# Kernel tuning notes

Measured on AMD Instinct MI355X. Metric: run time of the kernel, lower is better.

## Reference

```python
import jax, jax.numpy as jnp
import numpy as np
from jax import lax

# db4 analysis filters (pywt convention)
DEC_LO = np.array([-0.010597401785069032, 0.0328830116668852, 0.030841381835560764,
                   -0.18703481171909309, -0.027983769416859854, 0.6308807679298589,
                   0.7148465705529157, 0.2303778133088965], dtype=np.float32)
DEC_HI = np.array([-0.2303778133088965, 0.7148465705529157, -0.6308807679298589,
                   -0.027983769416859854, 0.18703481171909309, 0.030841381835560764,
                   -0.0328830116668852, -0.010597401785069032], dtype=np.float32)
LF = 8          # db4 filter length
J = 4           # wavelet levels
H = 768         # hidden size per modality
B, S = 8, 2048  # batch, seq len

# pytorch_wavelets cross-correlates with time-reversed dec filters (afb)
H0R = jnp.asarray(DEC_LO[::-1].copy())
H1R = jnp.asarray(DEC_HI[::-1].copy())
# conv_transpose(rec) == cross-correlation with flip(rec); flip(rec)=dec
G0F = jnp.asarray(DEC_LO)
G1F = jnp.asarray(DEC_HI)


def afb1d(x):
    """One analysis level along last axis, zero-pad mode. x: (B, C, N)."""
    b, c, n = x.shape
    outsize = (n + LF - 1) // 2          # pywt.dwt_coeff_len, mode='zero'
    p = 2 * (outsize - 1) - n + LF       # total pad (extra goes on the right)
    kern = jnp.stack([H0R, H1R])[:, None, :]               # (2,1,LF)
    y = lax.conv_general_dilated(x.reshape(b * c, 1, n), kern,
                                 (2,), [(p // 2, p - p // 2)])
    return y[:, 0].reshape(b, c, outsize), y[:, 1].reshape(b, c, outsize)


def sfb1d(lo, hi):
    """One synthesis level (inverse of afb1d). lo, hi: (B, C, N)."""
    b, c, n = lo.shape
    z = jnp.stack([lo.reshape(b * c, n), hi.reshape(b * c, n)], axis=1)  # (BC,2,N)
    kern = jnp.stack([G0F, G1F])[None]                     # (1,2,LF)
    # conv_transpose(stride=2, padding=LF-2) as lhs-dilated cross-correlation
    y = lax.conv_general_dilated(z, kern, (1,), [(1, 1)], lhs_dilation=(2,))
    return y[:, 0].reshape(b, c, 2 * n - LF + 2)


def dwt1d(x):
    highs = []
    lo = x
    for _ in range(J):
        lo, hi = afb1d(lo)
        highs.append(hi)
    return lo, highs


def idwt1d(lo, highs):
    for hi in highs[::-1]:
        if lo.shape[-1] > hi.shape[-1]:   # static shape check (as in IDWT1D)
            lo = lo[..., :-1]
        lo = sfb1d(lo, hi)
    return lo


def setup_inputs() -> dict:
    key = jax.random.key(0)
    k1, k2, k3 = jax.random.split(key, 3)
    x = jax.random.normal(k1, (B, S, 3 * H), dtype=jnp.float32)
    low_w = jax.random.normal(k2, (3, 3, H, H), dtype=jnp.float32) * 0.02
    high_w = jax.random.normal(k3, (3, J, 3, H, H), dtype=jnp.float32) * 0.02
    weight = jnp.ones((3,), dtype=jnp.float32)   # config['initializer_weight']
    return {"x": x, "low_w": low_w, "high_w": high_w, "weight": weight}


def reference(x, low_w, high_w, weight):
    b, s, _ = x.shape
    xs = jnp.stack(jnp.split(x, 3, axis=-1))               # (3,B,S,H) modalities
    xt = xs.transpose(0, 1, 3, 2).reshape(3 * b, H, s)     # DWT along seq axis
    lo, highs = dwt1d(xt)
    lo_s = lo.reshape(3, b, H, -1).transpose(0, 1, 3, 2)           # (3,B,Nl,H)
    hi_s = [h.reshape(3, b, H, -1).transpose(0, 1, 3, 2) for h in highs]

    # cross-modal sigmoid-gated fusion: m = target modal, j = source modal
    g = jnp.einsum('jbnh,mjgh->mjbng', lo_s, low_w)
    fused_l = (jax.nn.sigmoid(g) * lo_s[None]).sum(axis=1)         # (3,B,Nl,H)
    fused_h = []
    for k in range(J):
        gk = jnp.einsum('jbnh,mjgh->mjbng', hi_s[k], high_w[:, k])
        fused_h.append((jax.nn.sigmoid(gk) * hi_s[k][None]).sum(axis=1))

    fl = fused_l.transpose(0, 1, 3, 2).reshape(3 * b, H, -1)
    fh = [f.transpose(0, 1, 3, 2).reshape(3 * b, H, -1) for f in fused_h]
    recon = idwt1d(fl, fh).reshape(3, b, H, s).transpose(0, 1, 3, 2)  # (3,B,S,H)
    return (recon - xs) * weight[:, None, None, None]
```

## Files before the change

kernel.cpp:

```cpp
#include <hip/hip_runtime.h>
#include <hip/hip_bf16.h>

#define H 768
#define NB 8
#define SLEN 2048
#define N1 1027
#define N2 517
#define N3 262
#define N4 134

typedef short bf16x8 __attribute__((ext_vector_type(8)));
typedef float f32x4 __attribute__((ext_vector_type(4)));
typedef unsigned short ushortx4 __attribute__((ext_vector_type(4)));
typedef unsigned short ushortx8 __attribute__((ext_vector_type(8)));

__device__ __forceinline__ float sigmoidf(float v) {
    return 1.0f / (1.0f + __expf(-v));
}

__device__ __forceinline__ unsigned short f2bf(float f) {
    union { float f; unsigned u; } v; v.f = f;
    unsigned r = v.u + 0x7fffu + ((v.u >> 16) & 1u);
    return (unsigned short)(r >> 16);
}

__device__ __forceinline__ float bf2f(unsigned short u) {
    union { unsigned u; float f; } v; v.u = ((unsigned)u) << 16;
    return v.f;
}

__device__ __forceinline__ void gload_lds16(const void* g, void* l) {
    __builtin_amdgcn_global_load_lds(
        (const __attribute__((address_space(1))) unsigned int*)g,
        (__attribute__((address_space(3))) unsigned int*)l,
        16, 0, 0);
}

__global__ __launch_bounds__(192)
void dwt_analysis_kernel(const float* __restrict__ in,
                         float* __restrict__ lo_f32,
                         unsigned short* __restrict__ lo_bf,
                         unsigned short* __restrict__ hi_bf,
                         int n_in, int n_out, int rows_pad,
                         long j_stride, long b_stride, long t_stride)
{
    const float h0r[8] = { 0.2303778133088965f,  0.7148465705529157f,  0.6308807679298589f,
                          -0.027983769416859854f, -0.18703481171909309f, 0.030841381835560764f,
                           0.0328830116668852f, -0.010597401785069032f };
    const float h1r[8] = { -0.010597401785069032f, -0.0328830116668852f, 0.030841381835560764f,
                            0.18703481171909309f, -0.027983769416859854f, -0.6308807679298589f,
                            0.7148465705529157f, -0.2303778133088965f };
    const int tbase = blockIdx.x * 16;
    const int jb = blockIdx.y;
    const int j = jb >> 3, b = jb & 7;
    const int h = threadIdx.x * 4;
    const float* src = in + j * j_stride + b * b_stride + h;
    const float4 z4 = make_float4(0.f, 0.f, 0.f, 0.f);

    float4 w[8];
#pragma unroll
    for (int k = 0; k < 8; ++k) {
        int s = 2 * tbase - 6 + k;
        w[k] = (s >= 0 && s < n_in) ? *(const float4*)(src + (long)s * t_stride) : z4;
    }
#pragma unroll
    for (int tt = 0; tt < 16; ++tt) {
        const int t = tbase + tt;
        if (t < n_out) {
            float lx = 0.f, ly = 0.f, lz = 0.f, lw = 0.f;
            float hx = 0.f, hy = 0.f, hz = 0.f, hw = 0.f;
#pragma unroll
            for (int k = 0; k < 8; ++k) {
                float4 v = w[(2 * tt + k) & 7];
                lx += v.x * h0r[k]; ly += v.y * h0r[k]; lz += v.z * h0r[k]; lw += v.w * h0r[k];
                hx += v.x * h1r[k]; hy += v.y * h1r[k]; hz += v.z * h1r[k]; hw += v.w * h1r[k];
            }
            const long prow = (long)j * rows_pad + b * n_out + t;
            if (lo_f32) {
                float4 o; o.x = lx; o.y = ly; o.z = lz; o.w = lw;
                *(float4*)(lo_f32 + ((long)jb * n_out + t) * H + h) = o;
            }
            if (lo_bf) {
                ushortx4 p; p[0] = f2bf(lx); p[1] = f2bf(ly); p[2] = f2bf(lz); p[3] = f2bf(lw);
                *(ushortx4*)(lo_bf + prow * H + h) = p;
            }
            ushortx4 qv; qv[0] = f2bf(hx); qv[1] = f2bf(hy); qv[2] = f2bf(hz); qv[3] = f2bf(hw);
            *(ushortx4*)(hi_bf + prow * H + h) = qv;
        }
        if (tt < 15) {
            int s0n = 2 * t + 2;
            w[(2 * tt) & 7]     = (s0n     < n_in) ? *(const float4*)(src + (long)s0n * t_stride)       : z4;
            w[(2 * tt + 1) & 7] = (s0n + 1 < n_in) ? *(const float4*)(src + (long)(s0n + 1) * t_stride) : z4;
        }
    }
}

__device__ __forceinline__ void synth_pair(const float4* wl, const float4* wh, int u,
                                           float4* oe, float4* oo)
{
    const float g0[8] = { -0.010597401785069032f, 0.0328830116668852f, 0.030841381835560764f,
                          -0.18703481171909309f, -0.027983769416859854f, 0.6308807679298589f,
                           0.7148465705529157f, 0.2303778133088965f };
    const float g1[8] = { -0.2303778133088965f, 0.7148465705529157f, -0.6308807679298589f,
                          -0.027983769416859854f, 0.18703481171909309f, 0.030841381835560764f,
                          -0.0328830116668852f, -0.010597401785069032f };
    float ex = 0.f, ey = 0.f, ez = 0.f, ew = 0.f;
    float ox = 0.f, oy = 0.f, oz = 0.f, ow = 0.f;
#pragma unroll
    for (int d = 0; d < 4; ++d) {
        float4 vl = wl[(u + d) & 3];
        float4 vh = wh[(u + d) & 3];
        const float cle = g0[2 * d + 1], che = g1[2 * d + 1];
        const float clo = g0[2 * d],     cho = g1[2 * d];
        ex += vl.x * cle + vh.x * che; ey += vl.y * cle + vh.y * che;
        ez += vl.z * cle + vh.z * che; ew += vl.w * cle + vh.w * che;
        ox += vl.x * clo + vh.x * cho; oy += vl.y * clo + vh.y * cho;
        oz += vl.z * clo + vh.z * cho; ow += vl.w * clo + vh.w * cho;
    }
    oe->x = ex; oe->y = ey; oe->z = ez; oe->w = ew;
    oo->x = ox; oo->y = oy; oo->z = oz; oo->w = ow;
}

__global__ __launch_bounds__(192)
void dwt_synth_kernel(const float* __restrict__ lo,
                      const float* __restrict__ hi,
                      float* __restrict__ out,
                      int n, int lo_alloc, int n_out)
{
    const int ubase = blockIdx.x * 16;
    const int mb = blockIdx.y;
    const int h = threadIdx.x * 4;
    const float* lop = lo + (long)mb * lo_alloc * H + h;
    const float* hip_ = hi + (long)mb * n * H + h;
    float* outp = out + (long)mb * n_out * H + h;
    const float4 z4 = make_float4(0.f, 0.f, 0.f, 0.f);

    float4 wl[4], wh[4];
#pragma unroll
    for (int d = 0; d < 4; ++d) {
        int i = ubase + d;
        bool ok = (i < n);
        wl[(ubase + d) & 3] = ok ? *(const float4*)(lop + (long)i * H) : z4;
        wh[(ubase + d) & 3] = ok ? *(const float4*)(hip_ + (long)i * H) : z4;
    }
#pragma unroll
    for (int uu = 0; uu < 16; ++uu) {
        const int u = ubase + uu;
        if (2 * u < n_out) {
            float4 oe, oo;
            synth_pair(wl, wh, u, &oe, &oo);
            *(float4*)(outp + (long)(2 * u) * H) = oe;
            *(float4*)(outp + (long)(2 * u + 1) * H) = oo;
        }
        if (uu < 15) {
            int i = u + 4;
            bool ok = (i < n);
            wl[u & 3] = ok ? *(const float4*)(lop + (long)i * H) : z4;
            wh[u & 3] = ok ? *(const float4*)(hip_ + (long)i * H) : z4;
        }
    }
}

__global__ __launch_bounds__(192)
void dwt_synth_final_kernel(const float* __restrict__ lo,
                            const float* __restrict__ hi,
                            const float* __restrict__ x,
                            const float* __restrict__ weight,
                            float* __restrict__ out,
                            int n, int lo_alloc)
{
    const int ubase = blockIdx.x * 16;
    const int mb = blockIdx.y;
    const int m = mb >> 3, b = mb & 7;
    const int h = threadIdx.x * 4;
    const float* lop = lo + (long)mb * lo_alloc * H + h;
    const float* hip_ = hi + (long)mb * n * H + h;
    const float* xp = x + ((long)b * SLEN) * 2304 + (long)m * H + h;
    float* outp = out + (long)mb * SLEN * H + h;
    const float wgt = weight[m];
    const float4 z4 = make_float4(0.f, 0.f, 0.f, 0.f);

    float4 wl[4], wh[4];
#pragma unroll
    for (int d = 0; d < 4; ++d) {
        int i = ubase + d;
        bool ok = (i < n);
        wl[(ubase + d) & 3] = ok ? *(const float4*)(lop + (long)i * H) : z4;
        wh[(ubase + d) & 3] = ok ? *(const float4*)(hip_ + (long)i * H) : z4;
    }
#pragma unroll
    for (int uu = 0; uu < 16; ++uu) {
        const int u = ubase + uu;
        {
            float4 oe, oo;
            synth_pair(wl, wh, u, &oe, &oo);
            float4 xe = *(const float4*)(xp + (long)(2 * u) * 2304);
            float4 xo = *(const float4*)(xp + (long)(2 * u + 1) * 2304);
            float4 re, ro;
            re.x = (oe.x - xe.x) * wgt; re.y = (oe.y - xe.y) * wgt;
            re.z = (oe.z - xe.z) * wgt; re.w = (oe.w - xe.w) * wgt;
            ro.x = (oo.x - xo.x) * wgt; ro.y = (oo.y - xo.y) * wgt;
            ro.z = (oo.z - xo.z) * wgt; ro.w = (oo.w - xo.w) * wgt;
            *(float4*)(outp + (long)(2 * u) * H) = re;
            *(float4*)(outp + (long)(2 * u + 1) * H) = ro;
        }
        if (uu < 15) {
            int i = u + 4;
            bool ok = (i < n);
            wl[u & 3] = ok ? *(const float4*)(lop + (long)i * H) : z4;
            wh[u & 3] = ok ? *(const float4*)(hip_ + (long)i * H) : z4;
        }
    }
}

__global__ __launch_bounds__(256)
void cvt_weights_kernel(const float* __restrict__ low_w,
                        const float* __restrict__ high_w,
                        unsigned short* __restrict__ Wl,
                        unsigned short* __restrict__ Wh)
{
    const long HH = (long)H * H;
    const long nlow8 = 9L * HH / 8;
    const long total8 = 45L * HH / 8;
    long stride = (long)gridDim.x * blockDim.x;
    for (long idx = (long)blockIdx.x * blockDim.x + threadIdx.x; idx < total8; idx += stride) {
        const float* src;
        unsigned short* dst;
        if (idx < nlow8) { long e = idx * 8; src = low_w + e; dst = Wl + e; }
        else             { long e = (idx - nlow8) * 8; src = high_w + e; dst = Wh + e; }
        float4 a = *(const float4*)src;
        float4 b = *(const float4*)(src + 4);
        ushortx8 o;
        o[0] = f2bf(a.x); o[1] = f2bf(a.y); o[2] = f2bf(a.z); o[3] = f2bf(a.w);
        o[4] = f2bf(b.x); o[5] = f2bf(b.y); o[6] = f2bf(b.z); o[7] = f2bf(b.w);
        *(ushortx8*)dst = o;
    }
}

#define A1OFF 0L
#define A2OFF 19169280L
#define A3OFF 28901376L
#define A4OFF 33914880L
#define ALOFF 36569088L
#define WLOFF 39223296L
#define WHOFF 44531712L
#define F1OFF 0L
#define F2OFF 18929664L
#define F3OFF 28459008L
#define F4OFF 33288192L
#define FLOFF 35758080L
#define HHL (768L * 768L)

__global__ __launch_bounds__(512, 4)
void gating_mfma_kernel(const unsigned short* __restrict__ R2,
                        float* __restrict__ F0)
{
    __shared__ unsigned short ldsA[2][128 * 32];
    __shared__ unsigned short ldsB[2][128 * 32];
    const int tid = threadIdx.x;
    const int lane = tid & 63;
    const int wid = tid >> 6;
    const int wr = wid >> 2;
    const int wc = wid & 3;
    const int kq = lane >> 4;
    const int lr = lane & 15;

    const int nwg = 2394;
    const int orig = blockIdx.x;
    const int q = nwg >> 3, rm = nwg & 7;
    const int xcd = orig & 7, bidx = orig >> 3;
    const int swz = (xcd < rm) ? (xcd * (q + 1) + bidx)
                               : (rm * (q + 1) + (xcd - rm) * q + bidx);
    const int rt = swz / 18;
    const int ct = swz - rt * 18;
    const int m = ct / 6;
    const int gBlk = ct - m * 6;

    int rtl, rowsReal, rowsPad; long aOff, fOff, wOff, wm;
    if (rt < 65)       { rtl = rt;       rowsReal = 8216; rowsPad = 8320; aOff = A1OFF; fOff = F1OFF; wOff = WHOFF + 0 * 3 * HHL; wm = 12 * HHL; }
    else if (rt < 98)  { rtl = rt - 65;  rowsReal = 4136; rowsPad = 4224; aOff = A2OFF; fOff = F2OFF; wOff = WHOFF + 1 * 3 * HHL; wm = 12 * HHL; }
    else if (rt < 115) { rtl = rt - 98;  rowsReal = 2096; rowsPad = 2176; aOff = A3OFF; fOff = F3OFF; wOff = WHOFF + 2 * 3 * HHL; wm = 12 * HHL; }
    else if (rt < 124) { rtl = rt - 115; rowsReal = 1072; rowsPad = 1152; aOff = A4OFF; fOff = F4OFF; wOff = WHOFF + 3 * 3 * HHL; wm = 12 * HHL; }
    else               { rtl = rt - 124; rowsReal = 1072; rowsPad = 1152; aOff = ALOFF; fOff = FLOFF; wOff = WLOFF;              wm = 3 * HHL; }
    const int rowLocal = rtl * 128;

    const int gcol = gBlk * 128 + wc * 32;
    const int k0_g = gcol & ~63;
    const int kh_g = wc & 1;

    const int srow = wid * 16 + (lane >> 2);
    const int scol = 8 * ((lane & 3) ^ ((lane >> 3) & 3));

    const int sl = kq ^ ((lr >> 1) & 3);

    f32x4 fus[4][2], acc[4][2];
    unsigned gp[4][2][2];
#pragma unroll
    for (int a = 0; a < 4; ++a)
#pragma unroll
        for (int b = 0; b < 2; ++b) { fus[a][b] = (f32x4)0.f; acc[a][b] = (f32x4)0.f; }

    for (int j = 0; j < 3; ++j) {
        const unsigned short* A = R2 + aOff + (long)j * rowsPad * H;
        const unsigned short* W = R2 + wOff + (long)m * wm + (long)j * HHL;
        const unsigned short* Ag = A + (long)(rowLocal + srow) * H + scol;
        const unsigned short* Wg = W + (long)(gBlk * 128 + srow) * H + scol;

        for (int k0 = 0; k0 < H; k0 += 64) {
            __syncthreads();
            gload_lds16(Ag + k0,      (char*)&ldsA[0][0] + wid * 1024);
            gload_lds16(Ag + k0 + 32, (char*)&ldsA[1][0] + wid * 1024);
            gload_lds16(Wg + k0,      (char*)&ldsB[0][0] + wid * 1024);
            gload_lds16(Wg + k0 + 32, (char*)&ldsB[1][0] + wid * 1024);
            __syncthreads();

            if (k0 == k0_g) {
#pragma unroll
                for (int mi = 0; mi < 4; ++mi)
#pragma unroll
                    for (int ni = 0; ni < 2; ++ni)
#pragma unroll
                        for (int rp = 0; rp < 2; ++rp) {
                            const int rl = wr * 64 + mi * 16 + kq * 4 + rp * 2;
                            const int ec = ni * 16 + lr;
                            const int slotg = (ec >> 3) ^ ((kq * 2 + rp) & 3);
                            const int eoff = slotg * 8 + (ec & 7);
                            unsigned a0 = ldsA[kh_g][rl * 32 + eoff];
                            unsigned a1 = ldsA[kh_g][(rl + 1) * 32 + eoff];
                            gp[mi][ni][rp] = a0 | (a1 << 16);
                        }
            }

#pragma unroll
            for (int kh = 0; kh < 2; ++kh) {
                bf16x8 af[4], bfr[2];
#pragma unroll
                for (int mi = 0; mi < 4; ++mi)
                    af[mi] = *(const bf16x8*)&ldsA[kh][(wr * 64 + mi * 16 + lr) * 32 + sl * 8];
#pragma unroll
                for (int ni = 0; ni < 2; ++ni)
                    bfr[ni] = *(const bf16x8*)&ldsB[kh][(wc * 32 + ni * 16 + lr) * 32 + sl * 8];
#pragma unroll
                for (int mi = 0; mi < 4; ++mi)
#pragma unroll
                    for (int ni = 0; ni < 2; ++ni)
                        acc[mi][ni] = __builtin_amdgcn_mfma_f32_16x16x32_bf16(
                            af[mi], bfr[ni], acc[mi][ni], 0, 0, 0);
            }
        }

#pragma unroll
        for (int mi = 0; mi < 4; ++mi)
#pragma unroll
            for (int ni = 0; ni < 2; ++ni) {
#pragma unroll
                for (int rp = 0; rp < 2; ++rp) {
                    float c0 = bf2f((unsigned short)(gp[mi][ni][rp] & 0xffffu));
                    float c1 = bf2f((unsigned short)(gp[mi][ni][rp] >> 16));
                    fus[mi][ni][rp * 2]     += sigmoidf(acc[mi][ni][rp * 2])     * c0;
                    fus[mi][ni][rp * 2 + 1] += sigmoidf(acc[mi][ni][rp * 2 + 1]) * c1;
                }
                acc[mi][ni] = (f32x4)0.f;
            }
    }

    float* F = F0 + fOff;
#pragma unroll
    for (int mi = 0; mi < 4; ++mi)
#pragma unroll
        for (int ni = 0; ni < 2; ++ni)
#pragma unroll
            for (int reg = 0; reg < 4; ++reg) {
                const int rl = wr * 64 + mi * 16 + kq * 4 + reg;
                const int r = rowLocal + rl;
                if (r < rowsReal) {
                    const int g = gBlk * 128 + wc * 32 + ni * 16 + lr;
                    F[((long)m * rowsReal + r) * H + g] = fus[mi][ni][reg];
                }
            }
}

static inline int grid_for(long total) {
    long g = (total + 255) / 256;
    if (g > 16384) g = 16384;
    return (int)g;
}

extern "C" void kernel_launch(void* const* d_in, const int* in_sizes, int n_in,
                              void* d_out, int out_size, void* d_ws, size_t ws_size,
                              hipStream_t stream)
{
    const float* x      = (const float*)d_in[0];
    const float* low_w  = (const float*)d_in[1];
    const float* high_w = (const float*)d_in[2];
    const float* weight = (const float*)d_in[3];
    float* out = (float*)d_out;
    float* ws  = (float*)d_ws;

    const long HH = (long)H * H;
    const int rows1p = 8320, rows2p = 4224, rows3p = 2176, rows4p = 1152;

    float* B_lo1 = ws;
    float* B_lo2 = B_lo1 + 24L * N1 * H;
    float* B_lo3 = B_lo2 + 24L * N2 * H;
    float* F_hi1 = ws + F1OFF;
    float* F_hi2 = ws + F2OFF;
    float* F_hi3 = ws + F3OFF;
    float* F_hi4 = ws + F4OFF;
    float* F_lo  = ws + FLOFF;

    const long SZF = 24L * (N1 + N2 + N3 + 2 * N4) * H;
    float* R2f = ws + SZF;
    unsigned short* R2 = (unsigned short*)R2f;
    unsigned short* Abf1 = R2 + A1OFF;
    unsigned short* Abf2 = R2 + A2OFF;
    unsigned short* Abf3 = R2 + A3OFF;
    unsigned short* Abf4 = R2 + A4OFF;
    unsigned short* AbfL = R2 + ALOFF;
    unsigned short* Wl   = R2 + WLOFF;
    unsigned short* Wh   = R2 + WHOFF;
    float* Y1 = R2f;
    float* Y2 = Y1 + 24L * 262 * H;
    float* Y3 = Y2 + 24L * 518 * H;

    hipLaunchKernelGGL(dwt_analysis_kernel, dim3((N1 + 15) / 16, 24), dim3(192), 0, stream,
                       x, B_lo1, (unsigned short*)nullptr, Abf1,
                       SLEN, N1, rows1p, 768L, (long)SLEN * 2304, 2304L);
    hipLaunchKernelGGL(dwt_analysis_kernel, dim3((N2 + 15) / 16, 24), dim3(192), 0, stream,
                       B_lo1, B_lo2, (unsigned short*)nullptr, Abf2,
                       N1, N2, rows2p, 8L * N1 * H, (long)N1 * H, (long)H);
    hipLaunchKernelGGL(dwt_analysis_kernel, dim3((N3 + 15) / 16, 24), dim3(192), 0, stream,
                       B_lo2, B_lo3, (unsigned short*)nullptr, Abf3,
                       N2, N3, rows3p, 8L * N2 * H, (long)N2 * H, (long)H);
    hipLaunchKernelGGL(dwt_analysis_kernel, dim3((N4 + 15) / 16, 24), dim3(192), 0, stream,
                       B_lo3, (float*)nullptr, AbfL, Abf4,
                       N3, N4, rows4p, 8L * N3 * H, (long)N3 * H, (long)H);

    hipLaunchKernelGGL(cvt_weights_kernel, dim3(grid_for(45L * HH / 8)), dim3(256), 0, stream,
                       low_w, high_w, Wl, Wh);

    hipLaunchKernelGGL(gating_mfma_kernel, dim3(2394), dim3(512), 0, stream, R2, ws);

    hipLaunchKernelGGL(dwt_synth_kernel, dim3(9, 24), dim3(192), 0, stream,
                       F_lo, F_hi4, Y1, N4, N4, 262);
    hipLaunchKernelGGL(dwt_synth_kernel, dim3(17, 24), dim3(192), 0, stream,
                       Y1, F_hi3, Y2, N3, 262, 518);
    hipLaunchKernelGGL(dwt_synth_kernel, dim3(33, 24), dim3(192), 0, stream,
                       Y2, F_hi2, Y3, N2, 518, 1028);
    hipLaunchKernelGGL(dwt_synth_final_kernel, dim3(64, 24), dim3(192), 0, stream,
                       Y3, F_hi1, x, weight, out, N1, 1028);
}
```

Baseline: 608.8 us.

## Double-buffer LDS tiles in gating MFMA kernel with prefetch two stages ahead

Flattens the modality and K loops into a single 36-step fully unrolled loop and adds a second LDS buffer. Direct global-to-LDS loads for step t+2 are issued while step t computes, using vmcnt waits and raw s_barrier instead of full syncthreads. This is meant to hide global load latency behind MFMA work. LDS use doubles to 64KB per block, which may lower occupancy, and the full unroll increases code size and register pressure.

```diff
diff --git a/kernel.cpp b/kernel.cpp
--- a/kernel.cpp
+++ b/kernel.cpp
@@ -255,8 +255,8 @@
 void gating_mfma_kernel(const unsigned short* __restrict__ R2,
                         float* __restrict__ F0)
 {
-    __shared__ unsigned short ldsA[2][128 * 32];
-    __shared__ unsigned short ldsB[2][128 * 32];
+    __shared__ unsigned short ldsA[2][2][128 * 32];
+    __shared__ unsigned short ldsB[2][2][128 * 32];
     const int tid = threadIdx.x;
     const int lane = tid & 63;
     const int wid = tid >> 6;
@@ -293,6 +293,15 @@
 
     const int sl = kq ^ ((lr >> 1) & 3);
 
+    const unsigned short* Ag[3];
+    const unsigned short* Wg[3];
+    const unsigned short* Wb = R2 + wOff + (long)m * wm;
+#pragma unroll
+    for (int j = 0; j < 3; ++j) {
+        Ag[j] = R2 + aOff + (long)j * rowsPad * H + (long)(rowLocal + srow) * H + scol;
+        Wg[j] = Wb + (long)j * HHL + (long)(gBlk * 128 + srow) * H + scol;
+    }
+
     f32x4 fus[4][2], acc[4][2];
     unsigned gp[4][2][2];
 #pragma unroll
@@ -300,69 +309,87 @@
 #pragma unroll
         for (int b = 0; b < 2; ++b) { fus[a][b] = (f32x4)0.f; acc[a][b] = (f32x4)0.f; }
 
-    for (int j = 0; j < 3; ++j) {
-        const unsigned short* A = R2 + aOff + (long)j * rowsPad * H;
-        const unsigned short* W = R2 + wOff + (long)m * wm + (long)j * HHL;
-        const unsigned short* Ag = A + (long)(rowLocal + srow) * H + scol;
-        const unsigned short* Wg = W + (long)(gBlk * 128 + srow) * H + scol;
-
-        for (int k0 = 0; k0 < H; k0 += 64) {
-            __syncthreads();
-            gload_lds16(Ag + k0,      (char*)&ldsA[0][0] + wid * 1024);
-            gload_lds16(Ag + k0 + 32, (char*)&ldsA[1][0] + wid * 1024);
-            gload_lds16(Wg + k0,      (char*)&ldsB[0][0] + wid * 1024);
-            gload_lds16(Wg + k0 + 32, (char*)&ldsB[1][0] + wid * 1024);
-            __syncthreads();
-
-            if (k0 == k0_g) {
-#pragma unroll
-                for (int mi = 0; mi < 4; ++mi)
-#pragma unroll
-                    for (int ni = 0; ni < 2; ++ni)
-#pragma unroll
-                        for (int rp = 0; rp < 2; ++rp) {
-                            const int rl = wr * 64 + mi * 16 + kq * 4 + rp * 2;
-                            const int ec = ni * 16 + lr;
-                            const int slotg = (ec >> 3) ^ ((kq * 2 + rp) & 3);
-                            const int eoff = slotg * 8 + (ec & 7);
-                            unsigned a0 = ldsA[kh_g][rl * 32 + eoff];
-                            unsigned a1 = ldsA[kh_g][(rl + 1) * 32 + eoff];
-                            gp[mi][ni][rp] = a0 | (a1 << 16);
-                        }
-            }
-
-#pragma unroll
-            for (int kh = 0; kh < 2; ++kh) {
-                bf16x8 af[4], bfr[2];
-#pragma unroll
-                for (int mi = 0; mi < 4; ++mi)
-                    af[mi] = *(const bf16x8*)&ldsA[kh][(wr * 64 + mi * 16 + lr) * 32 + sl * 8];
+#define STAGE(buf, jj, kk) do {                                              \
+    gload_lds16(Ag[jj] + (kk),      (char*)&ldsA[buf][0][0] + wid * 1024);   \
+    gload_lds16(Ag[jj] + (kk) + 32, (char*)&ldsA[buf][1][0] + wid * 1024);   \
+    gload_lds16(Wg[jj] + (kk),      (char*)&ldsB[buf][0][0] + wid * 1024);   \
+    gload_lds16(Wg[jj] + (kk) + 32, (char*)&ldsB[buf][1][0] + wid * 1024);   \
+} while (0)
+
+    STAGE(0, 0, 0);
+    STAGE(1, 0, 64);
+
+#pragma unroll
+    for (int t = 0; t < 36; ++t) {
+        const int cur = t & 1;
+        const int j = t / 12;
+        const int kk0 = (t - j * 12) * 64;
+
+        if (t < 35) asm volatile("s_waitcnt vmcnt(4)" ::: "memory");
+        else        asm volatile("s_waitcnt vmcnt(0)" ::: "memory");
+        __builtin_amdgcn_s_barrier();
+
+        if (kk0 == k0_g) {
+            const unsigned short* gsrc = kh_g ? &ldsA[cur][1][0] : &ldsA[cur][0][0];
+#pragma unroll
+            for (int mi = 0; mi < 4; ++mi)
 #pragma unroll
                 for (int ni = 0; ni < 2; ++ni)
-                    bfr[ni] = *(const bf16x8*)&ldsB[kh][(wc * 32 + ni * 16 + lr) * 32 + sl * 8];
-#pragma unroll
-                for (int mi = 0; mi < 4; ++mi)
-#pragma unroll
-                    for (int ni = 0; ni < 2; ++ni)
-                        acc[mi][ni] = __builtin_amdgcn_mfma_f32_16x16x32_bf16(
-                            af[mi], bfr[ni], acc[mi][ni], 0, 0, 0);
-            }
-        }
-
-#pragma unroll
-        for (int mi = 0; mi < 4; ++mi)
-#pragma unroll
-            for (int ni = 0; ni < 2; ++ni) {
-#pragma unroll
-                for (int rp = 0; rp < 2; ++rp) {
-                    float c0 = bf2f((unsigned short)(gp[mi][ni][rp] & 0xffffu));
-                    float c1 = bf2f((unsigned short)(gp[mi][ni][rp] >> 16));
-                    fus[mi][ni][rp * 2]     += sigmoidf(acc[mi][ni][rp * 2])     * c0;
-                    fus[mi][ni][rp * 2 + 1] += sigmoidf(acc[mi][ni][rp * 2 + 1]) * c1;
+#pragma unroll
+                    for (int rp = 0; rp < 2; ++rp) {
+                        const int rl = wr * 64 + mi * 16 + kq * 4 + rp * 2;
+                        const int ec = ni * 16 + lr;
+                        const int slotg = (ec >> 3) ^ ((kq * 2 + rp) & 3);
+                        const int eoff = slotg * 8 + (ec & 7);
+                        unsigned a0 = gsrc[rl * 32 + eoff];
+                        unsigned a1 = gsrc[(rl + 1) * 32 + eoff];
+                        gp[mi][ni][rp] = a0 | (a1 << 16);
+                    }
+        }
+
+#pragma unroll
+        for (int kh = 0; kh < 2; ++kh) {
+            bf16x8 af[4], bfr[2];
+#pragma unroll
+            for (int mi = 0; mi < 4; ++mi)
+                af[mi] = *(const bf16x8*)&ldsA[cur][kh][(wr * 64 + mi * 16 + lr) * 32 + sl * 8];
+#pragma unroll
+            for (int ni = 0; ni < 2; ++ni)
+                bfr[ni] = *(const bf16x8*)&ldsB[cur][kh][(wc * 32 + ni * 16 + lr) * 32 + sl * 8];
+#pragma unroll
+            for (int mi = 0; mi < 4; ++mi)
+#pragma unroll
+                for (int ni = 0; ni < 2; ++ni)
+                    acc[mi][ni] = __builtin_amdgcn_mfma_f32_16x16x32_bf16(
+                        af[mi], bfr[ni], acc[mi][ni], 0, 0, 0);
+        }
+
+        if (t - j * 12 == 11) {
+#pragma unroll
+            for (int mi = 0; mi < 4; ++mi)
+#pragma unroll
+                for (int ni = 0; ni < 2; ++ni) {
+#pragma unroll
+                    for (int rp = 0; rp < 2; ++rp) {
+                        float c0 = bf2f((unsigned short)(gp[mi][ni][rp] & 0xffffu));
+                        float c1 = bf2f((unsigned short)(gp[mi][ni][rp] >> 16));
+                        fus[mi][ni][rp * 2]     += sigmoidf(acc[mi][ni][rp * 2])     * c0;
+                        fus[mi][ni][rp * 2 + 1] += sigmoidf(acc[mi][ni][rp * 2 + 1]) * c1;
+                    }
+                    acc[mi][ni] = (f32x4)0.f;
                 }
-                acc[mi][ni] = (f32x4)0.f;
-            }
-    }
+        }
+
+        asm volatile("" ::: "memory");
+        __builtin_amdgcn_s_barrier();
+        asm volatile("" ::: "memory");
+        if (t < 34) {
+            const int tp = t + 2;
+            const int jp = tp / 12;
+            STAGE(cur, jp, (tp - jp * 12) * 64);
+        }
+    }
+#undef STAGE
 
     float* F = F0 + fOff;
 #pragma unroll
```

New measurement: 601.1 us. Within noise of the previous version (-1.3%).
